# Kernel optimization log

Measured on AMD Instinct MI355X. Metric: run time of the kernel, lower is better.

## Reference

```python
import jax, jax.numpy as jnp
import numpy as np
import math

H, D_MODEL, D_C, D_ROPE = 16, 2048, 512, 64
D_HEAD = D_MODEL // H  # 128
D_QK = D_HEAD + D_ROPE  # 192


def precompute_freqs_cis(d_rope, seq_len, base=10000.0):
    # standard RoPE frequencies over pairs -> (seq_len, d_rope//2)
    inv_freq = 1.0 / (base ** (jnp.arange(0, d_rope, 2, dtype=jnp.float32) / d_rope))
    t = jnp.arange(seq_len, dtype=jnp.float32)
    ang = jnp.outer(t, inv_freq)
    return jnp.cos(ang), jnp.sin(ang)


def apply_rotary_emb(x, cos, sin):
    # x: (..., T, d_rope); cos/sin broadcastable (..., T, d_rope//2); interleaved pairs
    x1 = x[..., 0::2]
    x2 = x[..., 1::2]
    r1 = x1 * cos - x2 * sin
    r2 = x1 * sin + x2 * cos
    return jnp.stack([r1, r2], axis=-1).reshape(x.shape)


def setup_inputs() -> dict:
    key = jax.random.key(0)
    ks = jax.random.split(key, 10)
    B, T = 2, 2048
    s = 0.02
    return {
        "query": jax.random.normal(ks[0], (B, T, D_MODEL), jnp.float32),
        "key": jax.random.normal(ks[1], (B, T, D_MODEL), jnp.float32),
        "value": jax.random.normal(ks[2], (B, T, D_MODEL), jnp.float32),
        # weights stored (in_dim, out_dim)
        "W_DKV": jax.random.normal(ks[3], (D_MODEL, D_C), jnp.float32) * s,
        "W_UK": jax.random.normal(ks[4], (D_C, H * D_HEAD), jnp.float32) * s,
        "W_UV": jax.random.normal(ks[5], (D_C, H * D_HEAD), jnp.float32) * s,
        "W_Q": jax.random.normal(ks[6], (D_MODEL, H * D_HEAD), jnp.float32) * s,
        "W_KR": jax.random.normal(ks[7], (D_MODEL, D_ROPE), jnp.float32) * s,
        "W_QR": jax.random.normal(ks[8], (D_MODEL, H * D_ROPE), jnp.float32) * s,
        "W_O": jax.random.normal(ks[9], (H * D_HEAD, D_MODEL), jnp.float32) * s,
    }


def reference(query, key, value, W_DKV, W_UK, W_UV, W_Q, W_KR, W_QR, W_O):
    B, T_q, _ = query.shape
    T_k = key.shape[1]
    # low-rank latent KV compression
    c_kv = key @ W_DKV                                   # (B, Tk, d_c)
    k_nope = (c_kv @ W_UK).reshape(B, T_k, H, D_HEAD).transpose(0, 2, 1, 3)  # bhkd
    v = (c_kv @ W_UV).reshape(B, T_k, H, D_HEAD).transpose(0, 2, 1, 3)       # bhkd
    q_nope = (query @ W_Q).reshape(B, T_q, H, D_HEAD).transpose(0, 2, 1, 3)  # bhqd
    # decoupled RoPE subspace
    k_rope_in = (key @ W_KR)[:, None, :, :]              # (B,1,Tk,d_rope) shared across heads
    q_rope_in = (query @ W_QR).reshape(B, T_q, H, D_ROPE).transpose(0, 2, 1, 3)
    cos_q, sin_q = precompute_freqs_cis(D_ROPE, T_q)
    cos_k, sin_k = precompute_freqs_cis(D_ROPE, T_k)
    q_rope = apply_rotary_emb(q_rope_in, cos_q[None, None], sin_q[None, None])
    k_rope = apply_rotary_emb(k_rope_in, cos_k[None, None], sin_k[None, None])
    k_rope = jnp.broadcast_to(k_rope, (B, H, T_k, D_ROPE))
    # concat content + rope parts
    q = jnp.concatenate([q_nope, q_rope], axis=-1)       # (B,H,Tq,d_qk)
    k = jnp.concatenate([k_nope, k_rope], axis=-1)       # (B,H,Tk,d_qk)
    scores = jnp.einsum('bhqd,bhkd->bhqk', q, k) / math.sqrt(D_QK)
    p_attn = jax.nn.softmax(scores, axis=-1)             # dropout is identity (eval/p=0)
    x = jnp.einsum('bhqk,bhkd->bhqd', p_attn, v)
    x = x.transpose(0, 2, 1, 3).reshape(B, T_q, H * D_HEAD)
    output = x @ W_O
    return output, p_attn
```

## Files before the change

kernel.cpp:

```cpp
#include <hip/hip_runtime.h>
#include <hip/hip_bf16.h>
#include <math.h>

constexpr int B_   = 2;
constexpr int T_   = 2048;
constexpr int DM   = 2048;
constexpr int H_   = 16;
constexpr int DH   = 128;
constexpr int DC   = 512;
constexpr int DR   = 64;
constexpr int DQK  = DH + DR;
constexpr int BT   = B_ * T_;
constexpr int ZBH  = B_ * H_;

typedef __bf16 bf16x8 __attribute__((ext_vector_type(8)));
typedef float  f32x4  __attribute__((ext_vector_type(4)));
typedef unsigned int u32x2 __attribute__((ext_vector_type(2)));
typedef unsigned short u16x4 __attribute__((ext_vector_type(4)));

__device__ __forceinline__ unsigned pk2(float a, float b) {
  __hip_bfloat162 t = __float22bfloat162_rn(make_float2(a, b));
  return *reinterpret_cast<unsigned*>(&t);
}
__device__ __forceinline__ unsigned short bfbits(float v) {
  __hip_bfloat16 t = __float2bfloat16(v);
  return *reinterpret_cast<unsigned short*>(&t);
}

#define WAITVM(N)   asm volatile("s_waitcnt vmcnt(" #N ")" ::: "memory")
#define WAITVMLG(N) asm volatile("s_waitcnt vmcnt(" #N ") lgkmcnt(0)" ::: "memory")
#define BARSB() do { __builtin_amdgcn_s_barrier(); __builtin_amdgcn_sched_barrier(0); } while (0)
#define AS1 __attribute__((address_space(1)))
#define AS3 __attribute__((address_space(3)))

__global__ __launch_bounds__(256)
void prep(const float* __restrict__ query, const float* __restrict__ key,
          const float* __restrict__ W_Q, const float* __restrict__ W_QR,
          const float* __restrict__ W_DKV, const float* __restrict__ W_KR,
          const float* __restrict__ W_UK, const float* __restrict__ W_UV,
          const float* __restrict__ W_O,
          __hip_bfloat16* __restrict__ qB, __hip_bfloat16* __restrict__ kB,
          __hip_bfloat16* __restrict__ Wtqall, __hip_bfloat16* __restrict__ Wtkall,
          __hip_bfloat16* __restrict__ Wtkvup, __hip_bfloat16* __restrict__ WtO,
          float* __restrict__ ctab, float* __restrict__ stab) {
  __shared__ float tile[32][33];
  const int blk = blockIdx.x;
  const int tid = threadIdx.x;

  if (blk < 4096) {
    const float* src = (blk < 2048) ? query : key;
    __hip_bfloat16* dst = (blk < 2048) ? qB : kB;
    const long base = (long)(blk & 2047) * 4096;
    #pragma unroll
    for (int c = 0; c < 4; ++c) {
      const long off = base + c * 1024 + tid * 4;
      float4 f = *(const float4*)(src + off);
      u16x4 pk;
      pk[0] = bfbits(f.x); pk[1] = bfbits(f.y); pk[2] = bfbits(f.z); pk[3] = bfbits(f.w);
      *(u16x4*)(dst + off) = pk;
    }
    return;
  }

  int b = blk - 4096;
  const float* W = nullptr; __hip_bfloat16* Wt = nullptr; int K = 2048, N = 2048;
  if (b < 4096)               { W = W_Q;   Wt = Wtqall; }
  else if ((b -= 4096) < 2048){ W = W_QR;  Wt = Wtqall + (size_t)2048 * 2048; N = 1024; }
  else if ((b -= 2048) < 1024){ W = W_DKV; Wt = Wtkall; N = 512; }
  else if ((b -= 1024) < 128) { W = W_KR;  Wt = Wtkall + (size_t)512 * 2048; N = 64; }
  else if ((b -= 128) < 1024) { W = W_UK;  Wt = Wtkvup; K = 512; }
  else if ((b -= 1024) < 1024){ W = W_UV;  Wt = Wtkvup + (size_t)2048 * 512; K = 512; }
  else if ((b -= 1024) < 4096){ W = W_O;   Wt = WtO; }
  else {
    b -= 4096;
    const int i = b * 256 + tid;
    const int t = i >> 5, j = i & 31;
    double inv = pow(10000.0, -(double)j / 32.0);
    double ang = (double)t * inv;
    ctab[i] = (float)cos(ang);
    stab[i] = (float)sin(ang);
    return;
  }
  const int nx = N >> 5;
  const int n0 = (b % nx) << 5, k0 = (b / nx) << 5;
  const int tx = tid & 31, ty = tid >> 5;
  for (int i = ty; i < 32; i += 8)
    tile[i][tx] = W[(long)(k0 + i) * N + n0 + tx];
  __syncthreads();
  for (int i = ty; i < 32; i += 8)
    Wt[(long)(n0 + i) * K + k0 + tx] = __float2bfloat16(tile[tx][i]);
}

template <int MODE>
__global__ __launch_bounds__(512, 2)
void gemm_bt_256(const __hip_bfloat16* __restrict__ A, const __hip_bfloat16* __restrict__ Bt,
                 void* __restrict__ C0, void* __restrict__ C1,
                 int M, int N, int K, int lda,
                 const float* __restrict__ ctab, const float* __restrict__ stab) {
  const int gnx = N >> 8;
  const int nwg = (M >> 7) * gnx;
  const int cpx = nwg >> 3;
  const int bid = blockIdx.x;
  const int swz = (bid & 7) * cpx + (bid >> 3);
  const int n0 = (swz % gnx) << 8;
  const int m0 = (swz / gnx) << 7;

  __shared__ __align__(16) char lds[147456];

  const int tid  = threadIdx.x;
  const int wv   = tid >> 6;
  const int lane = tid & 63;
  const int wr   = wv >> 2;
  const int wc   = wv & 3;
  const int rr   = lane & 15;
  const int kq   = lane >> 4;

  const int cs16 = (((tid & 3) ^ ((tid >> 3) & 3)) << 4);
  const long arow  = m0 + (tid >> 2);
  const long brow0 = n0 + (tid >> 2);
  const long brow1 = n0 + 128 + (tid >> 2);

  auto stage = [&](int buf, int kh, int k0) {
    char* base = lds + buf * 49152 + kh * 24576;
    const long kk = (long)k0 + kh * 32;
    const char* asrc = (const char*)A + (arow * lda + kk) * 2 + cs16;
    __builtin_amdgcn_global_load_lds((const AS1 void*)asrc,
                                     (AS3 void*)(base + tid * 16), 16, 0, 0);
    const char* bsrc0 = (const char*)Bt + (brow0 * K + kk) * 2 + cs16;
    __builtin_amdgcn_global_load_lds((const AS1 void*)bsrc0,
                                     (AS3 void*)(base + 8192 + tid * 16), 16, 0, 0);
    const char* bsrc1 = (const char*)Bt + (brow1 * K + kk) * 2 + cs16;
    __builtin_amdgcn_global_load_lds((const AS1 void*)bsrc1,
                                     (AS3 void*)(base + 16384 + tid * 16), 16, 0, 0);
  };

  const int g16 = ((kq ^ ((rr >> 1) & 3)) << 4);
  const int aoff0 = (wr * 64 + rr) * 64 + g16;
  const int boff0 = 8192 + (wc * 64 + rr) * 64 + g16;

  f32x4 acc[4][4] = {};

  auto phase = [&](int buf, int kh) {
    char* base = lds + buf * 49152 + kh * 24576;
    bf16x8 a[4], b[4];
    #pragma unroll
    for (int mf = 0; mf < 4; ++mf) a[mf] = *(const bf16x8*)(base + aoff0 + mf * 1024);
    #pragma unroll
    for (int nf = 0; nf < 4; ++nf) b[nf] = *(const bf16x8*)(base + boff0 + nf * 1024);
    __builtin_amdgcn_s_setprio(1);
    #pragma unroll
    for (int mf = 0; mf < 4; ++mf)
      #pragma unroll
      for (int nf = 0; nf < 4; ++nf)
        acc[mf][nf] = __builtin_amdgcn_mfma_f32_16x16x32_bf16(a[mf], b[nf], acc[mf][nf], 0, 0, 0);
    __builtin_amdgcn_s_setprio(0);
  };

  const int NT = K >> 6;
  stage(0, 0, 0); stage(0, 1, 0);
  stage(1, 0, 64); stage(1, 1, 64);
  int cur = 0;
  for (int t = 0; t < NT; ++t) {
    const int b2 = (cur + 2 >= 3) ? cur - 1 : cur + 2;
    if (t + 2 < NT) {
      const int k2 = (t + 2) << 6;
      WAITVM(9);  BARSB();
      stage(b2, 0, k2);
      phase(cur, 0);
      WAITVM(9);  BARSB();
      stage(b2, 1, k2);
      phase(cur, 1);
    } else if (t + 2 == NT) {
      WAITVM(9);  BARSB();  phase(cur, 0);
      WAITVM(6);  BARSB();  phase(cur, 1);
    } else {
      WAITVM(3);  BARSB();  phase(cur, 0);
      WAITVM(0);  BARSB();  phase(cur, 1);
    }
    cur = (cur + 1 >= 3) ? 0 : cur + 1;
  }

  #pragma unroll
  for (int mf = 0; mf < 4; ++mf) {
    #pragma unroll
    for (int nf = 0; nf < 4; ++nf) {
      const int col = n0 + wc * 64 + nf * 16 + rr;
      const int rbase = m0 + wr * 64 + mf * 16 + kq * 4;
      if constexpr (MODE == 1) {
        float* C = (float*)C0;
        #pragma unroll
        for (int j = 0; j < 4; ++j)
          C[(long)(rbase + j) * N + col] = acc[mf][nf][j];
      } else if constexpr (MODE == 2) {
        __hip_bfloat16* qall = (__hip_bfloat16*)C0;
        if (col < 2048) {
          #pragma unroll
          for (int j = 0; j < 4; ++j)
            qall[(long)(rbase + j) * 3072 + col] = __float2bfloat16(acc[mf][nf][j]);
        } else {
          const int dr = (col - 2048) & 63;
          const int jj = dr >> 1;
          #pragma unroll
          for (int j = 0; j < 4; ++j) {
            const int row = rbase + j;
            const int t = row & (T_ - 1);
            const float c = ctab[t * 32 + jj], s = stab[t * 32 + jj];
            const float v  = acc[mf][nf][j];
            const float pv = __shfl_xor(v, 1);
            const float res = (dr & 1) ? (pv * s + v * c) : (v * c - pv * s);
            qall[(long)row * 3072 + col] = __float2bfloat16(res);
          }
        }
      } else if constexpr (MODE == 3) {
        __hip_bfloat16* ckv = (__hip_bfloat16*)C0;
        __hip_bfloat16* krp = (__hip_bfloat16*)C1;
        if (col < 512) {
          #pragma unroll
          for (int j = 0; j < 4; ++j)
            ckv[(long)(rbase + j) * 512 + col] = __float2bfloat16(acc[mf][nf][j]);
        } else if (col < 576) {
          const int dr = col - 512;
          const int jj = dr >> 1;
          #pragma unroll
          for (int j = 0; j < 4; ++j) {
            const int row = rbase + j;
            const int t = row & (T_ - 1);
            const float c = ctab[t * 32 + jj], s = stab[t * 32 + jj];
            const float v  = acc[mf][nf][j];
            const float pv = __shfl_xor(v, 1);
            const float res = (dr & 1) ? (pv * s + v * c) : (v * c - pv * s);
            krp[(long)row * 64 + dr] = __float2bfloat16(res);
          }
        }
      } else if constexpr (MODE == 4) {
        __hip_bfloat16* knope = (__hip_bfloat16*)C0;
        __hip_bfloat16* vT    = (__hip_bfloat16*)C1;
        if (col < 2048) {
          #pragma unroll
          for (int j = 0; j < 4; ++j)
            knope[(long)(rbase + j) * 2048 + col] = __float2bfloat16(acc[mf][nf][j]);
        } else {
          const int h = (col - 2048) >> 7, d = (col - 2048) & 127;
          const int z = (rbase >> 11) * 16 + h;
          const int t0 = rbase & (T_ - 1);
          u16x4 pk;
          #pragma unroll
          for (int j = 0; j < 4; ++j) pk[j] = bfbits(acc[mf][nf][j]);
          *(u16x4*)((__hip_bfloat16*)vT + ((long)z * DH + d) * T_ + t0) = pk;
        }
      }
    }
  }
}

__global__ __launch_bounds__(512)
void fused_attn(const __hip_bfloat16* __restrict__ q_all,
                const __hip_bfloat16* __restrict__ knope,
                const __hip_bfloat16* __restrict__ kroper,
                const __hip_bfloat16* __restrict__ vTg,
                float* __restrict__ patt,
                __hip_bfloat16* __restrict__ xplain) {
  constexpr int KT = 64;
  constexpr int NKT = T_ / KT;
  const int bid = blockIdx.x;
  const int swz = (bid & 7) * 64 + (bid >> 3);
  const int z  = swz >> 4;
  const int q0 = (swz & 15) << 7;
  const int b  = z >> 4, h = z & 15;
  const int tid  = threadIdx.x;
  const int wv   = tid >> 6;
  const int lane = tid & 63;
  const int rr   = lane & 15;
  const int kq   = lane >> 4;
  const float scl = 0.0721687836487032f;

  __shared__ __align__(16) char smem[81920];
  char* const lV = smem + 49152;
  char* const lP = smem + 65536;

  const long qrow = (long)(b * T_) + q0 + wv * 16 + rr;
  const __hip_bfloat16* qn = q_all + qrow * 3072 + h * 128;
  const __hip_bfloat16* qr = q_all + qrow * 3072 + 2048 + h * 64;
  bf16x8 qa[6];
  #pragma unroll
  for (int kc = 0; kc < 4; ++kc) qa[kc] = *(const bf16x8*)(qn + kc * 32 + kq * 8);
  #pragma unroll
  for (int kc = 0; kc < 2; ++kc) qa[4 + kc] = *(const bf16x8*)(qr + kc * 32 + kq * 8);

  auto stage_k = [&](char* dst, int kt0) {
    #pragma unroll
    for (int it = 0; it < 3; ++it) {
      const int off = it * 8192 + wv * 1024;
      const int lb  = off + lane * 16;
      const int row = lb / 384, cb = lb % 384;
      const int scb = cb ^ ((row & 7) << 4);
      const long trow = (long)(b * T_) + kt0 + row;
      const char* src = (scb < 256)
          ? (const char*)knope + trow * 4096 + h * 256 + scb
          : (const char*)kroper + trow * 128 + (scb - 256);
      __builtin_amdgcn_global_load_lds((const AS1 void*)src,
          (AS3 void*)(dst + off), 16, 0, 0);
    }
  };
  auto stage_v = [&](int kt0) {
    #pragma unroll
    for (int it = 0; it < 2; ++it) {
      const int off = it * 8192 + wv * 1024;
      const int lb  = off + lane * 16;
      const int row = lb >> 7, cb = lb & 127;
      const int scb = cb ^ ((row & 7) << 4);
      const char* src = (const char*)vTg + ((long)(z * DH + row) * T_ + kt0) * 2 + scb;
      __builtin_amdgcn_global_load_lds((const AS1 void*)src,
          (AS3 void*)(lV + off), 16, 0, 0);
    }
  };

  auto qkt = [&](const char* kb0, f32x4 (&sacc)[4]) {
    __builtin_amdgcn_s_setprio(1);
    #pragma unroll
    for (int kc = 0; kc < 6; ++kc) {
      #pragma unroll
      for (int n = 0; n < 4; ++n) {
        const int krow = n * 16 + rr;
        bf16x8 kb = *(const bf16x8*)(kb0 + krow * 384 +
                                     ((kc * 64 + kq * 16) ^ ((krow & 7) << 4)));
        sacc[n] = __builtin_amdgcn_mfma_f32_16x16x32_bf16(kb, qa[kc], sacc[n], 0, 0, 0);
      }
    }
    __builtin_amdgcn_s_setprio(0);
  };

  float mrun = -1e30f, srun = 0.f;

  stage_k(smem, 0);
  int cb3 = 0;
  for (int kt = 0; kt < NKT; ++kt) {
    const int nb3 = (cb3 + 1 == 3) ? 0 : cb3 + 1;
    if (kt + 1 < NKT) { stage_k(smem + nb3 * 24576, (kt + 1) * KT); WAITVM(3); }
    else WAITVM(0);
    BARSB();
    f32x4 sacc[4] = {};
    qkt(smem + cb3 * 24576, sacc);
    float tmax = sacc[0][0];
    #pragma unroll
    for (int n = 0; n < 4; ++n)
      #pragma unroll
      for (int r = 0; r < 4; ++r) tmax = fmaxf(tmax, sacc[n][r]);
    tmax = fmaxf(tmax, __shfl_xor(tmax, 16));
    tmax = fmaxf(tmax, __shfl_xor(tmax, 32));
    tmax *= scl;
    const float mnew = fmaxf(mrun, tmax);
    float ts = 0.f;
    #pragma unroll
    for (int n = 0; n < 4; ++n)
      #pragma unroll
      for (int r = 0; r < 4; ++r) ts += __expf(sacc[n][r] * scl - mnew);
    ts += __shfl_xor(ts, 16);
    ts += __shfl_xor(ts, 32);
    srun = srun * __expf(mrun - mnew) + ts;
    mrun = mnew;
    cb3 = nb3;
  }
  const float pis = 1.f / srun;
  BARSB();

  f32x4 oacc[8] = {};
  stage_k(smem, 0);
  int cur = 0;
  const int prow = wv * 16 + rr;
  for (int kt = 0; kt < NKT; ++kt) {
    const int kt0 = kt * KT;
    stage_v(kt0);
    if (kt + 1 < NKT) stage_k(smem + (cur ^ 1) * 24576, kt0 + KT);
    if (kt == 0)            WAITVM(5);
    else if (kt + 1 < NKT)  WAITVM(9);
    else                    WAITVM(6);
    BARSB();
    f32x4 sacc[4] = {};
    qkt(smem + cur * 24576, sacc);
    #pragma unroll
    for (int n = 0; n < 4; ++n) {
      f32x4 pv;
      #pragma unroll
      for (int r = 0; r < 4; ++r) pv[r] = __expf(sacc[n][r] * scl - mrun) * pis;
      __builtin_nontemporal_store(pv,
          (f32x4*)(patt + ((long)z * T_ + q0 + prow) * T_ + kt0 + n * 16 + kq * 4));
      u32x2 pw; pw[0] = pk2(pv[0], pv[1]); pw[1] = pk2(pv[2], pv[3]);
      *(u32x2*)(lP + prow * 128 + ((n * 32 + kq * 8) ^ ((prow & 7) << 4))) = pw;
    }
    if (kt + 1 < NKT) WAITVMLG(7); else WAITVMLG(4);
    BARSB();
    bf16x8 pa[2];
    #pragma unroll
    for (int kc = 0; kc < 2; ++kc)
      pa[kc] = *(const bf16x8*)(lP + prow * 128 + ((kc * 64 + kq * 16) ^ ((prow & 7) << 4)));
    __builtin_amdgcn_s_setprio(1);
    #pragma unroll
    for (int kc = 0; kc < 2; ++kc) {
      #pragma unroll
      for (int n = 0; n < 8; ++n) {
        const int vrow = n * 16 + rr;
        bf16x8 vb = *(const bf16x8*)(lV + vrow * 128 + ((kc * 64 + kq * 16) ^ ((vrow & 7) << 4)));
        oacc[n] = __builtin_amdgcn_mfma_f32_16x16x32_bf16(pa[kc], vb, oacc[n], 0, 0, 0);
      }
    }
    __builtin_amdgcn_s_setprio(0);
    BARSB();
    cur ^= 1;
  }

  #pragma unroll
  for (int n = 0; n < 8; ++n) {
    #pragma unroll
    for (int r = 0; r < 4; ++r) {
      const int q = q0 + wv * 16 + kq * 4 + r;
      xplain[((long)(b * T_ + q)) * DM + h * DH + n * 16 + rr] = __float2bfloat16(oacc[n][r]);
    }
  }
}

extern "C" void kernel_launch(void* const* d_in, const int* in_sizes, int n_in,
                              void* d_out, int out_size, void* d_ws, size_t ws_size,
                              hipStream_t stream) {
  const float* query = (const float*)d_in[0];
  const float* key   = (const float*)d_in[1];
  const float* W_DKV = (const float*)d_in[3];
  const float* W_UK  = (const float*)d_in[4];
  const float* W_UV  = (const float*)d_in[5];
  const float* W_Q   = (const float*)d_in[6];
  const float* W_KR  = (const float*)d_in[7];
  const float* W_QR  = (const float*)d_in[8];
  const float* W_O   = (const float*)d_in[9];

  float* out  = (float*)d_out;
  float* patt = out + (long)BT * DM;

  char* w = (char*)d_ws;
  auto alloc = [&](size_t bytes) { char* p = w; w += (bytes + 255) & ~(size_t)255; return p; };
  __hip_bfloat16* qB     = (__hip_bfloat16*)alloc((size_t)BT * DM * 2);
  __hip_bfloat16* kB     = (__hip_bfloat16*)alloc((size_t)BT * DM * 2);
  __hip_bfloat16* Wtqall = (__hip_bfloat16*)alloc((size_t)3072 * DM * 2);
  __hip_bfloat16* Wtkall = (__hip_bfloat16*)alloc((size_t)768 * DM * 2);
  __hip_bfloat16* Wtkvup = (__hip_bfloat16*)alloc((size_t)4096 * DC * 2);
  __hip_bfloat16* WtO    = (__hip_bfloat16*)alloc((size_t)DM * DM * 2);
  __hip_bfloat16* q_all  = (__hip_bfloat16*)alloc((size_t)BT * 3072 * 2);
  __hip_bfloat16* ckv    = (__hip_bfloat16*)alloc((size_t)BT * 512 * 2);
  __hip_bfloat16* kroper = (__hip_bfloat16*)alloc((size_t)BT * 64 * 2);
  __hip_bfloat16* knope  = (__hip_bfloat16*)alloc((size_t)BT * 2048 * 2);
  __hip_bfloat16* vT     = (__hip_bfloat16*)alloc((size_t)ZBH * DH * T_ * 2);
  __hip_bfloat16* xplain = (__hip_bfloat16*)alloc((size_t)BT * DM * 2);
  float*          ctab   = (float*)alloc((size_t)T_ * 32 * 4);
  float*          stab   = (float*)alloc((size_t)T_ * 32 * 4);

  hipMemsetAsync(Wtkall + (size_t)576 * DM, 0, (size_t)192 * DM * 2, stream);

  prep<<<dim3(17792), 256, 0, stream>>>(
      query, key, W_Q, W_QR, W_DKV, W_KR, W_UK, W_UV, W_O,
      qB, kB, Wtqall, Wtkall, Wtkvup, WtO, ctab, stab);

  gemm_bt_256<2><<<dim3(384), 512, 0, stream>>>(
      qB, Wtqall, q_all, nullptr, BT, 3072, DM, DM, ctab, stab);
  gemm_bt_256<3><<<dim3(96), 512, 0, stream>>>(
      kB, Wtkall, ckv, kroper, BT, 768, DM, DM, ctab, stab);
  gemm_bt_256<4><<<dim3(512), 512, 0, stream>>>(
      ckv, Wtkvup, knope, vT, BT, 4096, DC, 512, nullptr, nullptr);

  fused_attn<<<dim3(512), 512, 0, stream>>>(
      q_all, knope, kroper, vT, patt, xplain);

  gemm_bt_256<1><<<dim3(256), 512, 0, stream>>>(
      xplain, WtO, out, nullptr, BT, DM, DM, DM, nullptr, nullptr);
}
```

Baseline: 473.2 us.

## Deepen K/V prefetch pipelining in attention and fold memset into prep

In the attention kernel, the first (row-statistics) pass now uses four K buffers with a prefetch distance of two tiles, instead of three buffers with distance one. The second pass double-buffers both K and V, issuing the next tile's loads right after a single barrier, and drops the extra barriers around the P tile in LDS. Separately, the zeroing of the padded weight rows moves from a hipMemsetAsync into extra prep blocks, and the fp32 output GEMM now uses nontemporal stores. The aim is to hide global-load latency and cut synchronisation and launch overhead. The cost is that shared memory grows to 96KB, which may lower occupancy on the attention kernel.

```diff
diff --git a/kernel.cpp b/kernel.cpp
--- a/kernel.cpp
+++ b/kernel.cpp
@@ -28,7 +28,6 @@
 }
 
 #define WAITVM(N)   asm volatile("s_waitcnt vmcnt(" #N ")" ::: "memory")
-#define WAITVMLG(N) asm volatile("s_waitcnt vmcnt(" #N ") lgkmcnt(0)" ::: "memory")
 #define BARSB() do { __builtin_amdgcn_s_barrier(); __builtin_amdgcn_sched_barrier(0); } while (0)
 #define AS1 __attribute__((address_space(1)))
 #define AS3 __attribute__((address_space(3)))
@@ -71,8 +70,13 @@
   else if ((b -= 128) < 1024) { W = W_UK;  Wt = Wtkvup; K = 512; }
   else if ((b -= 1024) < 1024){ W = W_UV;  Wt = Wtkvup + (size_t)2048 * 512; K = 512; }
   else if ((b -= 1024) < 4096){ W = W_O;   Wt = WtO; }
+  else if ((b -= 4096) < 192) {
+    float4 z = {0.f, 0.f, 0.f, 0.f};
+    *(float4*)((char*)(Wtkall + (size_t)(576 + b) * 2048) + tid * 16) = z;
+    return;
+  }
   else {
-    b -= 4096;
+    b -= 192;
     const int i = b * 256 + tid;
     const int t = i >> 5, j = i & 31;
     double inv = pow(10000.0, -(double)j / 32.0);
@@ -190,7 +194,7 @@
         float* C = (float*)C0;
         #pragma unroll
         for (int j = 0; j < 4; ++j)
-          C[(long)(rbase + j) * N + col] = acc[mf][nf][j];
+          __builtin_nontemporal_store(acc[mf][nf][j], &C[(long)(rbase + j) * N + col]);
       } else if constexpr (MODE == 2) {
         __hip_bfloat16* qall = (__hip_bfloat16*)C0;
         if (col < 2048) {
@@ -274,9 +278,8 @@
   const int kq   = lane >> 4;
   const float scl = 0.0721687836487032f;
 
-  __shared__ __align__(16) char smem[81920];
-  char* const lV = smem + 49152;
-  char* const lP = smem + 65536;
+  __shared__ __align__(16) char smem[98304];
+  char* const lP = smem + 81920;
 
   const long qrow = (long)(b * T_) + q0 + wv * 16 + rr;
   const __hip_bfloat16* qn = q_all + qrow * 3072 + h * 128;
@@ -302,7 +305,7 @@
           (AS3 void*)(dst + off), 16, 0, 0);
     }
   };
-  auto stage_v = [&](int kt0) {
+  auto stage_v = [&](char* dst, int kt0) {
     #pragma unroll
     for (int it = 0; it < 2; ++it) {
       const int off = it * 8192 + wv * 1024;
@@ -311,7 +314,7 @@
       const int scb = cb ^ ((row & 7) << 4);
       const char* src = (const char*)vTg + ((long)(z * DH + row) * T_ + kt0) * 2 + scb;
       __builtin_amdgcn_global_load_lds((const AS1 void*)src,
-          (AS3 void*)(lV + off), 16, 0, 0);
+          (AS3 void*)(dst + off), 16, 0, 0);
     }
   };
 
@@ -333,14 +336,14 @@
   float mrun = -1e30f, srun = 0.f;
 
   stage_k(smem, 0);
-  int cb3 = 0;
+  stage_k(smem + 24576, KT);
   for (int kt = 0; kt < NKT; ++kt) {
-    const int nb3 = (cb3 + 1 == 3) ? 0 : cb3 + 1;
-    if (kt + 1 < NKT) { stage_k(smem + nb3 * 24576, (kt + 1) * KT); WAITVM(3); }
-    else WAITVM(0);
+    if (kt + 2 < NKT)      { stage_k(smem + ((kt + 2) & 3) * 24576, (kt + 2) * KT); WAITVM(6); }
+    else if (kt + 2 == NKT) WAITVM(3);
+    else                    WAITVM(0);
     BARSB();
     f32x4 sacc[4] = {};
-    qkt(smem + cb3 * 24576, sacc);
+    qkt(smem + (kt & 3) * 24576, sacc);
     float tmax = sacc[0][0];
     #pragma unroll
     for (int n = 0; n < 4; ++n)
@@ -359,25 +362,28 @@
     ts += __shfl_xor(ts, 32);
     srun = srun * __expf(mrun - mnew) + ts;
     mrun = mnew;
-    cb3 = nb3;
   }
   const float pis = 1.f / srun;
+
+  stage_k(smem, 0);
+  stage_v(smem + 49152, 0);
   BARSB();
 
   f32x4 oacc[8] = {};
-  stage_k(smem, 0);
+  const int prow = wv * 16 + rr;
   int cur = 0;
-  const int prow = wv * 16 + rr;
   for (int kt = 0; kt < NKT; ++kt) {
+    if (kt == 0) WAITVM(0); else WAITVM(4);
+    BARSB();
+    if (kt + 1 < NKT) {
+      stage_k(smem + (cur ? 0 : 24576), (kt + 1) * KT);
+      stage_v(smem + 49152 + (cur ? 0 : 16384), (kt + 1) * KT);
+    }
+    const char* lK = smem + (cur ? 24576 : 0);
+    const char* lV = smem + 49152 + (cur ? 16384 : 0);
+    f32x4 sacc[4] = {};
+    qkt(lK, sacc);
     const int kt0 = kt * KT;
-    stage_v(kt0);
-    if (kt + 1 < NKT) stage_k(smem + (cur ^ 1) * 24576, kt0 + KT);
-    if (kt == 0)            WAITVM(5);
-    else if (kt + 1 < NKT)  WAITVM(9);
-    else                    WAITVM(6);
-    BARSB();
-    f32x4 sacc[4] = {};
-    qkt(smem + cur * 24576, sacc);
     #pragma unroll
     for (int n = 0; n < 4; ++n) {
       f32x4 pv;
@@ -388,8 +394,6 @@
       u32x2 pw; pw[0] = pk2(pv[0], pv[1]); pw[1] = pk2(pv[2], pv[3]);
       *(u32x2*)(lP + prow * 128 + ((n * 32 + kq * 8) ^ ((prow & 7) << 4))) = pw;
     }
-    if (kt + 1 < NKT) WAITVMLG(7); else WAITVMLG(4);
-    BARSB();
     bf16x8 pa[2];
     #pragma unroll
     for (int kc = 0; kc < 2; ++kc)
@@ -405,7 +409,6 @@
       }
     }
     __builtin_amdgcn_s_setprio(0);
-    BARSB();
     cur ^= 1;
   }
 
@@ -452,9 +455,7 @@
   float*          ctab   = (float*)alloc((size_t)T_ * 32 * 4);
   float*          stab   = (float*)alloc((size_t)T_ * 32 * 4);
 
-  hipMemsetAsync(Wtkall + (size_t)576 * DM, 0, (size_t)192 * DM * 2, stream);
-
-  prep<<<dim3(17792), 256, 0, stream>>>(
+  prep<<<dim3(17984), 256, 0, stream>>>(
       query, key, W_Q, W_QR, W_DKV, W_KR, W_UK, W_UV, W_O,
       qB, kB, Wtqall, Wtkall, Wtkvup, WtO, ctab, stab);
 
```

New measurement: 440.9 us. -6.8%, faster.
